# Kernel optimization log

Hardware: AMD Instinct MI355X
Metric: run time of the kernel (lower is better)

The kernel has to match this reference:

```python
import jax, jax.numpy as jnp
import numpy as np
import math

B, S, HID = 2, 2048, 2048
NH, NKV, HD = 32, 8, 64
THETA = 10000.0
EPS = 1e-6
LAYER_IDX = 1
LAMBDA_INIT = 0.8 - 0.6 * math.exp(-0.3 * LAYER_IDX)
LAMBDA_STD = 0.1


def setup_inputs() -> dict:
    key = jax.random.key(0)
    ks = jax.random.split(key, 10)
    hidden_states = jax.random.normal(ks[0], (B, S, HID), jnp.float32)
    # RoPE cos/sin, llama convention: emb = cat(freqs, freqs)
    inv_freq = 1.0 / (THETA ** (np.arange(0, HD, 2, dtype=np.float32) / HD))
    freqs = np.outer(np.arange(S, dtype=np.float32), inv_freq)  # [S, HD/2]
    emb = np.concatenate([freqs, freqs], axis=-1)                # [S, HD]
    cos = jnp.broadcast_to(jnp.asarray(np.cos(emb), jnp.float32)[None], (B, S, HD))
    sin = jnp.broadcast_to(jnp.asarray(np.sin(emb), jnp.float32)[None], (B, S, HD))
    # additive causal mask [B,1,S,S]
    causal = jnp.triu(jnp.full((S, S), -1e9, dtype=jnp.float32), k=1)
    attention_mask = jnp.broadcast_to(causal[None, None], (B, 1, S, S))
    sc = 0.02
    wq = sc * jax.random.normal(ks[1], (NH * HD, HID), jnp.float32)
    wk = sc * jax.random.normal(ks[2], (NKV * HD, HID), jnp.float32)
    wv = sc * jax.random.normal(ks[3], (NKV * HD, HID), jnp.float32)
    wo = sc * jax.random.normal(ks[4], (HID, NH * HD), jnp.float32)
    lambda_q1 = LAMBDA_STD * jax.random.normal(ks[5], (HD,), jnp.float32)
    lambda_k1 = LAMBDA_STD * jax.random.normal(ks[6], (HD,), jnp.float32)
    lambda_q2 = LAMBDA_STD * jax.random.normal(ks[7], (HD,), jnp.float32)
    lambda_k2 = LAMBDA_STD * jax.random.normal(ks[8], (HD,), jnp.float32)
    return {"hidden_states": hidden_states, "cos": cos, "sin": sin,
            "attention_mask": attention_mask, "wq": wq, "wk": wk, "wv": wv,
            "wo": wo, "lambda_q1": lambda_q1, "lambda_k1": lambda_k1,
            "lambda_q2": lambda_q2, "lambda_k2": lambda_k2}


def _rotate_half(x):
    x1, x2 = jnp.split(x, 2, axis=-1)
    return jnp.concatenate([-x2, x1], axis=-1)


def reference(hidden_states, cos, sin, attention_mask, wq, wk, wv, wo,
              lambda_q1, lambda_k1, lambda_q2, lambda_k2):
    b, s, _ = hidden_states.shape
    # projections -> [b, h, s, d]
    q = jnp.einsum('bsh,oh->bso', hidden_states, wq).reshape(b, s, NH, HD).transpose(0, 2, 1, 3)
    k = jnp.einsum('bsh,oh->bso', hidden_states, wk).reshape(b, s, NKV, HD).transpose(0, 2, 1, 3)
    v = jnp.einsum('bsh,oh->bso', hidden_states, wv).reshape(b, s, NKV, HD).transpose(0, 2, 1, 3)
    # rotary
    c, sn = cos[:, None], sin[:, None]  # [b,1,s,d]
    q = q * c + _rotate_half(q) * sn
    k = k * c + _rotate_half(k) * sn
    # GQA repeat
    groups = NH // NKV
    k = jnp.repeat(k, groups, axis=1)
    v = jnp.repeat(v, groups, axis=1)
    # diff-attention value trick: pair head i with head i+NH/2 -> [b, NH, s, 2d]
    v = jnp.concatenate([v[:, :NH // 2], v[:, NH // 2:]], axis=-1)  # [b, NH/2, s, 2d]
    v = jnp.concatenate([v, v], axis=1)                              # [b, NH, s, 2d]
    # scores + causal mask, stable softmax in fp32
    aw = jnp.einsum('bhqd,bhkd->bhqk', q, k) / math.sqrt(HD)
    aw = aw + attention_mask
    aw = jax.nn.softmax(aw.astype(jnp.float32), axis=-1).astype(q.dtype)
    ao = jnp.einsum('bhqk,bhkd->bhqd', aw, v)  # [b, NH, s, 2d]
    lam1 = jnp.exp(jnp.sum((lambda_q1 * lambda_k1).astype(jnp.float32)))
    lam2 = jnp.exp(jnp.sum((lambda_q2 * lambda_k2).astype(jnp.float32)))
    lam = (lam1 - lam2).astype(q.dtype) + LAMBDA_INIT
    a1, a2 = ao[:, :NH // 2], ao[:, NH // 2:]
    out = a1 - lam * a2  # [b, NH/2, s, 2d]
    # RMSNorm over last dim (no affine)
    out = out * jax.lax.rsqrt(jnp.mean(out * out, axis=-1, keepdims=True) + EPS)
    out = (1.0 - LAMBDA_INIT) * out
    out = out.transpose(0, 2, 1, 3).reshape(b, s, NH * HD)
    return jnp.einsum('bso,ho->bsh', out, wo)
```

## Files before the change

### kernel.cpp

```cpp
#include <hip/hip_runtime.h>

typedef __attribute__((ext_vector_type(8))) short bhalf8;
typedef __attribute__((ext_vector_type(4))) float floatx4;

constexpr int B_ = 2, S_ = 2048, HID_ = 2048, NH_ = 32, NKV_ = 8, HD_ = 64;
constexpr float LAMBDA_INIT_F = 0.35550906759096924f;
constexpr float EPS_ = 1e-6f;
constexpr float QSCALE_ = 0.18033688011112042f;

#define DEVINL __device__ __forceinline__

DEVINL float bf2f(unsigned short u) {
    union { unsigned u; float f; } v; v.u = ((unsigned)u) << 16; return v.f;
}
DEVINL unsigned short f2bf(float f) {
    union { float f; unsigned u; } v; v.f = f;
    unsigned u = v.u;
    return (unsigned short)((u + 0x7fffu + ((u >> 16) & 1u)) >> 16);
}
DEVINL float fexp2(float x) {
#if __has_builtin(__builtin_amdgcn_exp2f)
    return __builtin_amdgcn_exp2f(x);
#else
    return exp2f(x);
#endif
}
DEVINL unsigned pk_bf16(float a, float b) {
#if __has_builtin(__builtin_amdgcn_cvt_pk_bf16_f32)
    typedef __bf16 bf16x2_t __attribute__((ext_vector_type(2)));
    bf16x2_t p = __builtin_amdgcn_cvt_pk_bf16_f32(a, b);
    unsigned r;
    __builtin_memcpy(&r, &p, 4);
    return r;
#else
    return (unsigned)f2bf(a) | ((unsigned)f2bf(b) << 16);
#endif
}
DEVINL void load_lds16(const unsigned short* g, unsigned short* l) {
    __builtin_amdgcn_global_load_lds(
        (const __attribute__((address_space(1))) unsigned int*)g,
        (__attribute__((address_space(3))) unsigned int*)l, 16, 0, 0);
}

__global__ __launch_bounds__(256)
void cvt_all(const float* __restrict__ hs, const float* __restrict__ wq,
             const float* __restrict__ wk, const float* __restrict__ wv,
             const float* __restrict__ wo, unsigned short* __restrict__ hs_bf,
             unsigned short* __restrict__ wcat, unsigned short* __restrict__ wo_bf) {
    const size_t i = (size_t)(blockIdx.x * 256 + threadIdx.x) * 4;
    const float* src;
    unsigned short* dst;
    size_t off;
    float scale = 1.f;
    if (i < 8388608) { src = hs; dst = hs_bf; off = 0; }
    else if (i < 12582912) { src = wq; dst = wcat; off = 8388608; scale = QSCALE_; }
    else if (i < 13631488) { src = wk; dst = wcat + 4194304; off = 12582912; }
    else if (i < 14680064) { src = wv; dst = wcat + 5242880; off = 13631488; }
    else { src = wo; dst = wo_bf; off = 14680064; }
    const size_t k = i - off;
    const float4 v = *(const float4*)(src + k);
    ushort4 o;
    o.x = f2bf(v.x * scale); o.y = f2bf(v.y * scale);
    o.z = f2bf(v.z * scale); o.w = f2bf(v.w * scale);
    *(ushort4*)(dst + k) = o;
}

__global__ void lam_kernel(const float* __restrict__ q1, const float* __restrict__ k1,
                           const float* __restrict__ q2, const float* __restrict__ k2,
                           float* __restrict__ lam) {
    const int l = threadIdx.x;
    float p1 = q1[l] * k1[l];
    float p2 = q2[l] * k2[l];
    #pragma unroll
    for (int off = 1; off < 64; off <<= 1) {
        p1 += __shfl_xor(p1, off, 64);
        p2 += __shfl_xor(p2, off, 64);
    }
    if (l == 0) *lam = expf(p1) - expf(p2) + LAMBDA_INIT_F;
}

__global__ __launch_bounds__(256)
void gemm_qkv(const unsigned short* __restrict__ A, const unsigned short* __restrict__ Bw,
              const float* __restrict__ cosb, const float* __restrict__ sinb,
              unsigned short* __restrict__ Qr, unsigned short* __restrict__ Kr,
              unsigned short* __restrict__ VT) {
    constexpr int K = 2048;
    union GS {
        struct { unsigned short A[2][128][32]; unsigned short B[2][128][32]; } d;
        unsigned short vt[128][130];
    };
    __shared__ __align__(16) GS gsm;
    const int t = threadIdx.x;
    const int w = t >> 6, lane = t & 63, quad = lane >> 4, lid = lane & 15;
    const int wr = (w >> 1) * 64, wc = (w & 1) * 64;
    const long bm = (long)blockIdx.x * 128, bn = (long)blockIdx.y * 128;

    floatx4 acc[4][4];
    #pragma unroll
    for (int i = 0; i < 4; i++)
        #pragma unroll
        for (int j = 0; j < 4; j++) acc[i][j] = (floatx4){0.f, 0.f, 0.f, 0.f};

    const int s0 = t, s1 = t + 256;
    const unsigned short* Ag0 = A + (bm + (s0 >> 2)) * (long)K + (s0 & 3) * 8;
    const unsigned short* Ag1 = A + (bm + (s1 >> 2)) * (long)K + (s1 & 3) * 8;
    const unsigned short* Bg0 = Bw + (bn + (s0 >> 2)) * (long)K + (s0 & 3) * 8;
    const unsigned short* Bg1 = Bw + (bn + (s1 >> 2)) * (long)K + (s1 & 3) * 8;
    const int l0 = s0 * 8, l1 = s1 * 8;

    load_lds16(Ag0, &gsm.d.A[0][0][0] + l0);
    load_lds16(Ag1, &gsm.d.A[0][0][0] + l1);
    load_lds16(Bg0, &gsm.d.B[0][0][0] + l0);
    load_lds16(Bg1, &gsm.d.B[0][0][0] + l1);
    __syncthreads();

    const int nk = K >> 5;
    for (int kt = 0; kt < nk; kt++) {
        const int cur = kt & 1, nxt = cur ^ 1;
        if (kt + 1 < nk) {
            const int off = (kt + 1) << 5;
            load_lds16(Ag0 + off, &gsm.d.A[nxt][0][0] + l0);
            load_lds16(Ag1 + off, &gsm.d.A[nxt][0][0] + l1);
            load_lds16(Bg0 + off, &gsm.d.B[nxt][0][0] + l0);
            load_lds16(Bg1 + off, &gsm.d.B[nxt][0][0] + l1);
        }
        bhalf8 af[4], bf[4];
        #pragma unroll
        for (int i = 0; i < 4; i++) af[i] = *(const bhalf8*)&gsm.d.A[cur][wr + i * 16 + lid][quad * 8];
        #pragma unroll
        for (int j = 0; j < 4; j++) bf[j] = *(const bhalf8*)&gsm.d.B[cur][wc + j * 16 + lid][quad * 8];
        #pragma unroll
        for (int i = 0; i < 4; i++)
            #pragma unroll
            for (int j = 0; j < 4; j++)
                acc[i][j] = __builtin_amdgcn_mfma_f32_16x16x32_bf16(af[i], bf[j], acc[i][j], 0, 0, 0);
        __syncthreads();
    }

    const int y = blockIdx.y;
    if (y < 20) {
        const bool isQ = (y < 16);
        #pragma unroll
        for (int i = 0; i < 4; i++) {
            #pragma unroll
            for (int r = 0; r < 4; r++) {
                const long row = bm + wr + i * 16 + quad * 4 + r;
                const int bb = (int)(row >> 11), s = (int)(row & 2047);
                const float* cp = cosb + (size_t)row * 64;
                const float* sp = sinb + (size_t)row * 64;
                #pragma unroll
                for (int jj = 0; jj < 4; jj++) {
                    const int col = (int)bn + wc + jj * 16 + lid;
                    const int d = col & 63;
                    const float x = acc[i][jj][r];
                    const float oth = acc[i][jj ^ 2][r];
                    const float rot = (jj < 2) ? -oth : oth;
                    const float yv = x * cp[d] + rot * sp[d];
                    if (isQ) {
                        const int h = col >> 6;
                        Qr[((size_t)(bb * NH_ + h) * S_ + s) * HD_ + d] = f2bf(yv);
                    } else {
                        const int h = (col - 2048) >> 6;
                        Kr[((size_t)(bb * NKV_ + h) * S_ + s) * HD_ + d] = f2bf(yv);
                    }
                }
            }
        }
    } else {
        #pragma unroll
        for (int i = 0; i < 4; i++)
            #pragma unroll
            for (int jj = 0; jj < 4; jj++)
                #pragma unroll
                for (int r = 0; r < 4; r++)
                    gsm.vt[wr + i * 16 + quad * 4 + r][wc + jj * 16 + lid] = f2bf(acc[i][jj][r]);
        __syncthreads();
        const int b0 = (int)(bm >> 11), sbase = (int)(bm & 2047);
        #pragma unroll 4
        for (int it = 0; it < 32; it++) {
            const int d = w + 4 * it;
            const int colg = (int)bn + d;
            const int h = (colg - 2560) >> 6;
            const int dl = colg & 63;
            const int sl = lane * 2;
            const unsigned v = (unsigned)gsm.vt[sl][d] | ((unsigned)gsm.vt[sl + 1][d] << 16);
            *(unsigned*)(VT + ((size_t)(b0 * NKV_ + h) * HD_ + dl) * S_ + sbase + sl) = v;
        }
    }
}

__global__ __launch_bounds__(256)
void gemm_bt(const unsigned short* __restrict__ A, const unsigned short* __restrict__ Bw,
             float* __restrict__ Cout, int M, int N, int K) {
    __shared__ __align__(16) unsigned short As[2][128][32];
    __shared__ __align__(16) unsigned short Bs[2][128][32];
    const int t = threadIdx.x;
    const int w = t >> 6, lane = t & 63, quad = lane >> 4, lid = lane & 15;
    const int wr = (w >> 1) * 64, wc = (w & 1) * 64;
    const long bm = (long)blockIdx.x * 128, bn = (long)blockIdx.y * 128;

    floatx4 acc[4][4];
    #pragma unroll
    for (int i = 0; i < 4; i++)
        #pragma unroll
        for (int j = 0; j < 4; j++) acc[i][j] = (floatx4){0.f, 0.f, 0.f, 0.f};

    const int s0 = t, s1 = t + 256;
    const unsigned short* Ag0 = A + (bm + (s0 >> 2)) * (long)K + (s0 & 3) * 8;
    const unsigned short* Ag1 = A + (bm + (s1 >> 2)) * (long)K + (s1 & 3) * 8;
    const unsigned short* Bg0 = Bw + (bn + (s0 >> 2)) * (long)K + (s0 & 3) * 8;
    const unsigned short* Bg1 = Bw + (bn + (s1 >> 2)) * (long)K + (s1 & 3) * 8;
    const int l0 = s0 * 8, l1 = s1 * 8;

    load_lds16(Ag0, &As[0][0][0] + l0);
    load_lds16(Ag1, &As[0][0][0] + l1);
    load_lds16(Bg0, &Bs[0][0][0] + l0);
    load_lds16(Bg1, &Bs[0][0][0] + l1);
    __syncthreads();

    const int nk = K >> 5;
    for (int kt = 0; kt < nk; kt++) {
        const int cur = kt & 1, nxt = cur ^ 1;
        if (kt + 1 < nk) {
            const int off = (kt + 1) << 5;
            load_lds16(Ag0 + off, &As[nxt][0][0] + l0);
            load_lds16(Ag1 + off, &As[nxt][0][0] + l1);
            load_lds16(Bg0 + off, &Bs[nxt][0][0] + l0);
            load_lds16(Bg1 + off, &Bs[nxt][0][0] + l1);
        }
        bhalf8 af[4], bf[4];
        #pragma unroll
        for (int i = 0; i < 4; i++) af[i] = *(const bhalf8*)&As[cur][wr + i * 16 + lid][quad * 8];
        #pragma unroll
        for (int j = 0; j < 4; j++) bf[j] = *(const bhalf8*)&Bs[cur][wc + j * 16 + lid][quad * 8];
        #pragma unroll
        for (int i = 0; i < 4; i++)
            #pragma unroll
            for (int j = 0; j < 4; j++)
                acc[i][j] = __builtin_amdgcn_mfma_f32_16x16x32_bf16(af[i], bf[j], acc[i][j], 0, 0, 0);
        __syncthreads();
    }

    #pragma unroll
    for (int i = 0; i < 4; i++) {
        #pragma unroll
        for (int j = 0; j < 4; j++) {
            const long row = bm + wr + i * 16 + quad * 4;
            const long col = bn + wc + j * 16 + lid;
            #pragma unroll
            for (int r = 0; r < 4; r++) Cout[(row + r) * N + col] = acc[i][j][r];
        }
    }
}

__global__ __launch_bounds__(512, 4)
void attn_diff(const unsigned short* __restrict__ Qr, const unsigned short* __restrict__ Kr,
               const unsigned short* __restrict__ VT, const float* __restrict__ lamp,
               unsigned short* __restrict__ attn) {
    union SM {
        struct {
            unsigned short Kt[2][64][72];
            unsigned short Vt[128][72];
            unsigned short Pt[8][16][72];
        } a;
        unsigned short Ot[2][64][132];
    };
    __shared__ __align__(16) SM sm;

    const int j = blockIdx.y, b = blockIdx.z;
    const int t = threadIdx.x;
    const int w = t >> 6, lane = t & 63, quad = lane >> 4, lid = lane & 15;
    const int st = w >> 2;
    const int rh = (w & 3) * 16;
    const int kv1 = j >> 2, kv2 = 4 + (j >> 2);
    const int qhead = j + st * 16;
    const float lam = *lamp;

    const int ss = t >> 8, kidx = t & 255;
    const int key_s = kidx >> 2, dh = (kidx & 3) * 16;
    const unsigned short* ksrc0 = Kr + (size_t)(b * NKV_ + (ss ? kv2 : kv1)) * S_ * HD_ +
                                  (size_t)key_s * HD_ + dh;
    const int d7 = t >> 2, vh = (t & 3) * 16;
    const unsigned short* vsrc0 = VT + ((size_t)(b * NKV_ + (d7 < 64 ? kv1 : kv2)) * HD_ +
                                        (d7 & 63)) * (size_t)S_ + vh;

    for (int half = 0; half < 2; half++) {
        const int qt = half ? (31 - (int)blockIdx.x) : (int)blockIdx.x;
        const int qb = qt * 64;

        const unsigned short* qbase =
            Qr + ((size_t)((b * NH_ + qhead) * S_) + qb + rh + lid) * HD_;
        const bhalf8 qa0 = *(const bhalf8*)(qbase + quad * 8);
        const bhalf8 qa1 = *(const bhalf8*)(qbase + 32 + quad * 8);

        floatx4 acc[8];
        #pragma unroll
        for (int c = 0; c < 8; c++) acc[c] = (floatx4){0.f, 0.f, 0.f, 0.f};
        float l_acc[4] = {0.f, 0.f, 0.f, 0.f};

        const int nkt = qt + 1;

        int4 kr0 = *(const int4*)(ksrc0);
        int4 kr1 = *(const int4*)(ksrc0 + 8);
        int4 vr0 = *(const int4*)(vsrc0);
        int4 vr1 = *(const int4*)(vsrc0 + 8);

        for (int kt = 0; kt < nkt; kt++) {
            asm volatile("s_waitcnt vmcnt(0)" ::: "memory");
            __builtin_amdgcn_s_barrier();
            __builtin_amdgcn_sched_barrier(0);
            *(int4*)&sm.a.Kt[ss][key_s][dh] = kr0;
            *(int4*)&sm.a.Kt[ss][key_s][dh + 8] = kr1;
            *(int4*)&sm.a.Vt[d7][vh] = vr0;
            *(int4*)&sm.a.Vt[d7][vh + 8] = vr1;
            if (kt + 1 < nkt) {
                const unsigned short* kp = ksrc0 + (size_t)(kt + 1) * 64 * HD_;
                const unsigned short* vp = vsrc0 + (kt + 1) * 64;
                kr0 = *(const int4*)(kp);
                kr1 = *(const int4*)(kp + 8);
                vr0 = *(const int4*)(vp);
                vr1 = *(const int4*)(vp + 8);
            }
            asm volatile("s_waitcnt lgkmcnt(0)" ::: "memory");
            __builtin_amdgcn_s_barrier();
            __builtin_amdgcn_sched_barrier(0);

            const bool last = (kt == nkt - 1);
            const int nt_lim = last ? ((w & 3) + 1) : 4;

            floatx4 sc[4];
            __builtin_amdgcn_s_setprio(1);
            #pragma unroll
            for (int nt = 0; nt < 4; nt++) {
                if (nt < nt_lim) {
                    const bhalf8 kb0 = *(const bhalf8*)&sm.a.Kt[st][nt * 16 + lid][quad * 8];
                    const bhalf8 kb1 = *(const bhalf8*)&sm.a.Kt[st][nt * 16 + lid][32 + quad * 8];
                    floatx4 z = (floatx4){0.f, 0.f, 0.f, 0.f};
                    z = __builtin_amdgcn_mfma_f32_16x16x32_bf16(qa0, kb0, z, 0, 0, 0);
                    z = __builtin_amdgcn_mfma_f32_16x16x32_bf16(qa1, kb1, z, 0, 0, 0);
                    sc[nt] = z;
                }
            }
            __builtin_amdgcn_s_setprio(0);

            if (last) {
                #pragma unroll
                for (int nt = 0; nt < 4; nt++) {
                    const int keyg = kt * 64 + nt * 16 + lid;
                    #pragma unroll
                    for (int r = 0; r < 4; r++) {
                        float p = 0.f;
                        if (nt < nt_lim) {
                            const int rowg = qb + rh + quad * 4 + r;
                            p = (keyg > rowg) ? 0.f : fexp2(sc[nt][r]);
                        }
                        sc[nt][r] = p;
                        l_acc[r] += p;
                    }
                }
            } else {
                #pragma unroll
                for (int nt = 0; nt < 4; nt++)
                    #pragma unroll
                    for (int r = 0; r < 4; r++) {
                        const float p = fexp2(sc[nt][r]);
                        sc[nt][r] = p;
                        l_acc[r] += p;
                    }
            }

            #pragma unroll
            for (int nt = 0; nt < 4; nt++) {
                #pragma unroll
                for (int r = 0; r < 4; r += 2) {
                    const unsigned pk = pk_bf16(sc[nt][r], sc[nt][r + 1]);
                    sm.a.Pt[w][quad * 4 + r][nt * 16 + lid] = (unsigned short)(pk & 0xffff);
                    sm.a.Pt[w][quad * 4 + r + 1][nt * 16 + lid] = (unsigned short)(pk >> 16);
                }
            }

            __builtin_amdgcn_s_setprio(1);
            #pragma unroll
            for (int kk = 0; kk < 2; kk++) {
                if (nt_lim > kk * 2) {
                    const bhalf8 pa = *(const bhalf8*)&sm.a.Pt[w][lid][kk * 32 + quad * 8];
                    #pragma unroll
                    for (int c = 0; c < 8; c++) {
                        const bhalf8 vb = *(const bhalf8*)&sm.a.Vt[c * 16 + lid][kk * 32 + quad * 8];
                        acc[c] = __builtin_amdgcn_mfma_f32_16x16x32_bf16(pa, vb, acc[c], 0, 0, 0);
                    }
                }
            }
            __builtin_amdgcn_s_setprio(0);
        }

        #pragma unroll
        for (int off = 1; off < 16; off <<= 1)
            #pragma unroll
            for (int r = 0; r < 4; r++) l_acc[r] += __shfl_xor(l_acc[r], off, 64);

        __syncthreads();
        #pragma unroll
        for (int r = 0; r < 4; r++) {
            const float rl = 1.0f / l_acc[r];
            #pragma unroll
            for (int c = 0; c < 8; c++)
                sm.Ot[st][rh + quad * 4 + r][c * 16 + lid] = f2bf(acc[c][r] * rl);
        }
        __syncthreads();

        const int row = t >> 3, m = t & 7;
        float vals[16];
        float ssum = 0.f;
        #pragma unroll
        for (int c = 0; c < 4; c++) {
            const unsigned long long u0 = *(const unsigned long long*)&sm.Ot[0][row][m * 4 + 32 * c];
            const unsigned long long u1 = *(const unsigned long long*)&sm.Ot[1][row][m * 4 + 32 * c];
            #pragma unroll
            for (int i = 0; i < 4; i++) {
                const float x = bf2f((unsigned short)(u0 >> (16 * i))) -
                                lam * bf2f((unsigned short)(u1 >> (16 * i)));
                vals[c * 4 + i] = x;
                ssum += x * x;
            }
        }
        ssum += __shfl_xor(ssum, 1, 64);
        ssum += __shfl_xor(ssum, 2, 64);
        ssum += __shfl_xor(ssum, 4, 64);
        const float scale = (1.f - LAMBDA_INIT_F) * rsqrtf(ssum * (1.f / 128.f) + EPS_);
        unsigned short* dst = attn + (size_t)(b * S_ + qb + row) * (NH_ * HD_) + j * 128 + m * 4;
        #pragma unroll
        for (int c = 0; c < 4; c++) {
            unsigned short ob[4];
            #pragma unroll
            for (int i = 0; i < 4; i++) ob[i] = f2bf(vals[c * 4 + i] * scale);
            *(unsigned long long*)(dst + 32 * c) = *(const unsigned long long*)ob;
        }
        __syncthreads();
    }
}

extern "C" void kernel_launch(void* const* d_in, const int* in_sizes, int n_in,
                              void* d_out, int out_size, void* d_ws, size_t ws_size,
                              hipStream_t stream) {
    const float* hs   = (const float*)d_in[0];
    const float* cosb = (const float*)d_in[1];
    const float* sinb = (const float*)d_in[2];
    const float* wq   = (const float*)d_in[4];
    const float* wk   = (const float*)d_in[5];
    const float* wv   = (const float*)d_in[6];
    const float* wo   = (const float*)d_in[7];
    const float* lq1  = (const float*)d_in[8];
    const float* lk1  = (const float*)d_in[9];
    const float* lq2  = (const float*)d_in[10];
    const float* lk2  = (const float*)d_in[11];

    unsigned short* p = (unsigned short*)d_ws;
    unsigned short* hs_bf = p;  p += (size_t)4096 * 2048;
    unsigned short* wcat  = p;  p += (size_t)3072 * 2048;
    unsigned short* wo_bf = p;  p += (size_t)2048 * 2048;
    unsigned short* Qr    = p;  p += (size_t)B_ * NH_ * S_ * HD_;
    unsigned short* Kr    = p;  p += (size_t)B_ * NKV_ * S_ * HD_;
    unsigned short* VT    = p;  p += (size_t)B_ * NKV_ * S_ * HD_;
    unsigned short* attnb = p;  p += (size_t)4096 * 2048;
    float* lam = (float*)p;

    cvt_all<<<18432, 256, 0, stream>>>(hs, wq, wk, wv, wo, hs_bf, wcat, wo_bf);
    lam_kernel<<<1, 64, 0, stream>>>(lq1, lk1, lq2, lk2, lam);
    gemm_qkv<<<dim3(32, 24), 256, 0, stream>>>(hs_bf, wcat, cosb, sinb, Qr, Kr, VT);
    attn_diff<<<dim3(16, 16, 2), 512, 0, stream>>>(Qr, Kr, VT, lam, attnb);
    gemm_bt<<<dim3(32, 16), 256, 0, stream>>>(attnb, wo_bf, (float*)d_out, 4096, 2048, 2048);
}
```

Before: 351.9 us.

## Transpose attention MFMAs and pass P fragments via ds_bpermute instead of LDS

The QK^T and PV MFMAs now run with swapped operands, so each lane holds scores for one query row across four keys. The softmax probabilities are packed to bf16 and redistributed between lanes with ds_bpermute into the B-operand layout, which removes the Pt shared-memory staging buffer along with its scattered 16-bit stores and reloads. The row sum becomes a single per-lane scalar reduced over quads, and the output tile is written to LDS as packed 64-bit stores. In exchange it adds cross-lane permute instructions and selects, and the new lane-mapping arithmetic is easy to get wrong.

```diff
diff --git a/kernel.cpp b/kernel.cpp
--- a/kernel.cpp
+++ b/kernel.cpp
@@ -40,6 +40,9 @@
     __builtin_amdgcn_global_load_lds(
         (const __attribute__((address_space(1))) unsigned int*)g,
         (__attribute__((address_space(3))) unsigned int*)l, 16, 0, 0);
+}
+DEVINL unsigned bper(unsigned v, int byteidx) {
+    return (unsigned)__builtin_amdgcn_ds_bpermute(byteidx, (int)v);
 }
 
 __global__ __launch_bounds__(256)
@@ -261,7 +264,6 @@
         struct {
             unsigned short Kt[2][64][72];
             unsigned short Vt[128][72];
-            unsigned short Pt[8][16][72];
         } a;
         unsigned short Ot[2][64][132];
     };
@@ -275,6 +277,9 @@
     const int kv1 = j >> 2, kv2 = 4 + (j >> 2);
     const int qhead = j + st * 16;
     const float lam = *lamp;
+    const bool hiq = (quad >= 2);
+    const int bq0 = ((((2 * quad) & 3) * 16 + lid) << 2);
+    const int bq1 = bq0 + 64;
 
     const int ss = t >> 8, kidx = t & 255;
     const int key_s = kidx >> 2, dh = (kidx & 3) * 16;
@@ -296,7 +301,7 @@
         floatx4 acc[8];
         #pragma unroll
         for (int c = 0; c < 8; c++) acc[c] = (floatx4){0.f, 0.f, 0.f, 0.f};
-        float l_acc[4] = {0.f, 0.f, 0.f, 0.f};
+        float lsum = 0.f;
 
         const int nkt = qt + 1;
 
@@ -327,6 +332,7 @@
 
             const bool last = (kt == nkt - 1);
             const int nt_lim = last ? ((w & 3) + 1) : 4;
+            const int k0 = kt * 64;
 
             floatx4 sc[4];
             __builtin_amdgcn_s_setprio(1);
@@ -336,26 +342,26 @@
                     const bhalf8 kb0 = *(const bhalf8*)&sm.a.Kt[st][nt * 16 + lid][quad * 8];
                     const bhalf8 kb1 = *(const bhalf8*)&sm.a.Kt[st][nt * 16 + lid][32 + quad * 8];
                     floatx4 z = (floatx4){0.f, 0.f, 0.f, 0.f};
-                    z = __builtin_amdgcn_mfma_f32_16x16x32_bf16(qa0, kb0, z, 0, 0, 0);
-                    z = __builtin_amdgcn_mfma_f32_16x16x32_bf16(qa1, kb1, z, 0, 0, 0);
+                    z = __builtin_amdgcn_mfma_f32_16x16x32_bf16(kb0, qa0, z, 0, 0, 0);
+                    z = __builtin_amdgcn_mfma_f32_16x16x32_bf16(kb1, qa1, z, 0, 0, 0);
                     sc[nt] = z;
                 }
             }
             __builtin_amdgcn_s_setprio(0);
 
             if (last) {
+                const int rowg = qb + rh + lid;
                 #pragma unroll
                 for (int nt = 0; nt < 4; nt++) {
-                    const int keyg = kt * 64 + nt * 16 + lid;
                     #pragma unroll
                     for (int r = 0; r < 4; r++) {
                         float p = 0.f;
                         if (nt < nt_lim) {
-                            const int rowg = qb + rh + quad * 4 + r;
+                            const int keyg = k0 + nt * 16 + quad * 4 + r;
                             p = (keyg > rowg) ? 0.f : fexp2(sc[nt][r]);
                         }
                         sc[nt][r] = p;
-                        l_acc[r] += p;
+                        lsum += p;
                     }
                 }
             } else {
@@ -365,47 +371,57 @@
                     for (int r = 0; r < 4; r++) {
                         const float p = fexp2(sc[nt][r]);
                         sc[nt][r] = p;
-                        l_acc[r] += p;
+                        lsum += p;
                     }
             }
 
-            #pragma unroll
-            for (int nt = 0; nt < 4; nt++) {
-                #pragma unroll
-                for (int r = 0; r < 4; r += 2) {
-                    const unsigned pk = pk_bf16(sc[nt][r], sc[nt][r + 1]);
-                    sm.a.Pt[w][quad * 4 + r][nt * 16 + lid] = (unsigned short)(pk & 0xffff);
-                    sm.a.Pt[w][quad * 4 + r + 1][nt * 16 + lid] = (unsigned short)(pk >> 16);
-                }
+            bhalf8 pfrag[2];
+            #pragma unroll
+            for (int m = 0; m < 2; m++) {
+                const unsigned a0 = pk_bf16(sc[2 * m][0], sc[2 * m][1]);
+                const unsigned a1 = pk_bf16(sc[2 * m][2], sc[2 * m][3]);
+                const unsigned b0 = pk_bf16(sc[2 * m + 1][0], sc[2 * m + 1][1]);
+                const unsigned b1 = pk_bf16(sc[2 * m + 1][2], sc[2 * m + 1][3]);
+                const unsigned pa0 = bper(a0, bq0), pb0 = bper(b0, bq0);
+                const unsigned pa1 = bper(a1, bq0), pb1 = bper(b1, bq0);
+                const unsigned qa0_ = bper(a0, bq1), qb0_ = bper(b0, bq1);
+                const unsigned qa1_ = bper(a1, bq1), qb1_ = bper(b1, bq1);
+                unsigned du[4];
+                du[0] = hiq ? pb0 : pa0;
+                du[1] = hiq ? pb1 : pa1;
+                du[2] = hiq ? qb0_ : qa0_;
+                du[3] = hiq ? qb1_ : qa1_;
+                __builtin_memcpy(&pfrag[m], du, 16);
             }
 
             __builtin_amdgcn_s_setprio(1);
             #pragma unroll
             for (int kk = 0; kk < 2; kk++) {
                 if (nt_lim > kk * 2) {
-                    const bhalf8 pa = *(const bhalf8*)&sm.a.Pt[w][lid][kk * 32 + quad * 8];
                     #pragma unroll
                     for (int c = 0; c < 8; c++) {
                         const bhalf8 vb = *(const bhalf8*)&sm.a.Vt[c * 16 + lid][kk * 32 + quad * 8];
-                        acc[c] = __builtin_amdgcn_mfma_f32_16x16x32_bf16(pa, vb, acc[c], 0, 0, 0);
+                        acc[c] = __builtin_amdgcn_mfma_f32_16x16x32_bf16(vb, pfrag[kk], acc[c], 0, 0, 0);
                     }
                 }
             }
             __builtin_amdgcn_s_setprio(0);
         }
 
-        #pragma unroll
-        for (int off = 1; off < 16; off <<= 1)
-            #pragma unroll
-            for (int r = 0; r < 4; r++) l_acc[r] += __shfl_xor(l_acc[r], off, 64);
-
-        __syncthreads();
-        #pragma unroll
-        for (int r = 0; r < 4; r++) {
-            const float rl = 1.0f / l_acc[r];
-            #pragma unroll
-            for (int c = 0; c < 8; c++)
-                sm.Ot[st][rh + quad * 4 + r][c * 16 + lid] = f2bf(acc[c][r] * rl);
+        lsum += __shfl_xor(lsum, 16, 64);
+        lsum += __shfl_xor(lsum, 32, 64);
+
+        __syncthreads();
+        {
+            const float rl = 1.0f / lsum;
+            #pragma unroll
+            for (int c = 0; c < 8; c++) {
+                const unsigned p01 = pk_bf16(acc[c][0] * rl, acc[c][1] * rl);
+                const unsigned p23 = pk_bf16(acc[c][2] * rl, acc[c][3] * rl);
+                const unsigned long long u =
+                    (unsigned long long)p01 | ((unsigned long long)p23 << 32);
+                *(unsigned long long*)&sm.Ot[st][rh + lid][c * 16 + quad * 4] = u;
+            }
         }
         __syncthreads();
 
```

Measured after the change: 360.8 us. 2.5% more time.
